# Kernel optimization log

Hardware: AMD Instinct MI355X
Metric: run time of the kernel (lower is better)

The kernel has to match this reference:

```python
import jax, jax.numpy as jnp
import numpy as np
import math

B, S, HID = 1, 4096, 2048
NH, NKV, HD = 16, 4, 128
SKETCH, TOPK = 640, 2048
EPS = 1e-6


def _dct_orthonormal(rows, cols, rng, sink=4, fsink=8):
    i = np.arange(rows)[:, None]
    j = np.arange(cols)[None, :]
    dct = np.cos(np.pi / cols * (j + 0.5) * i)
    dct[0, :] *= math.sqrt(1.0 / cols)
    dct[1:, :] *= math.sqrt(2.0 / cols)
    signs = rng.integers(0, 2, (1, cols)).astype(np.float64) * 2.0 - 1.0
    m = dct * signs
    m[:, :sink] *= 2.0
    m[:fsink, :] *= 1.5
    return m.astype(np.float32)


def setup_inputs() -> dict:
    key = jax.random.key(0)
    ks = jax.random.split(key, 8)
    rng = np.random.default_rng(0)
    # RoPE tables (b, s, 1, head_dim)
    pos = np.arange(S, dtype=np.float32)
    inv = 1.0 / (10000.0 ** (np.arange(0, HD, 2, dtype=np.float32) / HD))
    ang = pos[:, None] * inv[None, :]              # (S, HD/2)
    emb = np.concatenate([ang, ang], axis=-1)       # (S, HD)
    cos = np.broadcast_to(np.cos(emb)[None, :, None, :], (B, S, 1, HD)).copy()
    sin = np.broadcast_to(np.sin(emb)[None, :, None, :], (B, S, 1, HD)).copy()
    w = 0.02
    return {
        'hidden_states': jax.random.normal(ks[0], (B, S, HID), jnp.float32),
        'wq': jax.random.normal(ks[1], (HID, NH * HD), jnp.float32) * w,
        'wk': jax.random.normal(ks[2], (HID, NKV * HD), jnp.float32) * w,
        'wv': jax.random.normal(ks[3], (HID, NKV * HD), jnp.float32) * w,
        'wo': jax.random.normal(ks[4], (NH * HD, HID), jnp.float32) * w,
        'qn_w': jnp.ones((HD,), jnp.float32),
        'kn_w': jnp.ones((HD,), jnp.float32),
        's_w1': jax.random.normal(ks[5], (HID, 64), jnp.float32) * w,
        's_b1': jnp.zeros((64,), jnp.float32),
        's_w2': jax.random.normal(ks[6], (64, 1), jnp.float32) * w,
        's_b2': jnp.zeros((1,), jnp.float32),
        'sketch_scale': jnp.full((1,), 0.1, jnp.float32),
        'kron_a': jnp.asarray(_dct_orthonormal(20, 128, rng)),
        'kron_b': jnp.asarray(_dct_orthonormal(32, 256, rng)),
        'cos': jnp.asarray(cos),
        'sin': jnp.asarray(sin),
    }


def _rms_norm(x, w):
    var = jnp.mean(jnp.square(x), axis=-1, keepdims=True)
    return x * jax.lax.rsqrt(var + EPS) * w


def _rope(x, cos, sin):
    # x: (b, s, h, d); cos/sin: (b, s, 1, d)
    d2 = x.shape[-1] // 2
    rot = jnp.concatenate([-x[..., d2:], x[..., :d2]], axis=-1)
    return x * cos + rot * sin


def reference(hidden_states, wq, wk, wv, wo, qn_w, kn_w, s_w1, s_b1, s_w2, s_b2,
              sketch_scale, kron_a, kron_b, cos, sin):
    b, s, _ = hidden_states.shape
    # importance scorer with compression pressure bias
    logits = jnp.tanh(hidden_states @ s_w1 + s_b1) @ s_w2 + s_b2   # (b, s, 1)
    if s > SKETCH:
        logits = logits - math.log(s / SKETCH)
    iw = jax.nn.sigmoid(logits)                                    # (b, s, 1)

    q = (hidden_states @ wq).reshape(b, s, NH, HD)
    k = (hidden_states @ wk).reshape(b, s, NKV, HD)
    v = (hidden_states @ wv).reshape(b, s, NKV, HD)
    q = _rms_norm(q, qn_w)
    k = _rms_norm(k, kn_w)

    tk = min(s, TOPK)
    _, idx = jax.lax.top_k(logits[..., 0], tk)                     # (b, tk)
    ix = idx[:, :, None, None]
    k_detail = jnp.take_along_axis(k, ix, axis=1)                  # (b, tk, nkv, d)
    v_detail = jnp.take_along_axis(v, ix, axis=1)
    cos_det = jnp.take_along_axis(cos, ix, axis=1)                 # (b, tk, 1, d)
    sin_det = jnp.take_along_axis(sin, ix, axis=1)

    # Kronecker sketch of importance-weighted K/V over all tokens
    P = jnp.kron(kron_a, kron_b)[:, :s]                            # (640, s)
    kw = k * iw[..., None]
    vw = v * iw[..., None]
    k_sketch = jnp.einsum('bshd,ms->bmhd', kw, P) * sketch_scale
    v_sketch = jnp.einsum('bshd,ms->bmhd', vw, P) * sketch_scale

    q_rope = _rope(q, cos, sin)
    k_detail = _rope(k_detail, cos_det, sin_det)

    k_final = jnp.concatenate([k_detail, k_sketch], axis=1)        # (b, tk+640, nkv, d)
    v_final = jnp.concatenate([v_detail, v_sketch], axis=1)
    rep = NH // NKV
    k_final = jnp.repeat(k_final, rep, axis=2)                     # (b, L, nh, d)
    v_final = jnp.repeat(v_final, rep, axis=2)

    scores = jnp.einsum('bqhd,bkhd->bhqk', q_rope, k_final) / math.sqrt(HD)
    attn = jax.nn.softmax(scores, axis=-1)
    out = jnp.einsum('bhqk,bkhd->bqhd', attn, v_final).reshape(b, s, NH * HD)
    return out @ wo
```

## Files before the change

### kernel.cpp

```cpp
#include <hip/hip_runtime.h>
#include <math.h>

typedef _Float16 f16;
typedef f16 f16x8 __attribute__((ext_vector_type(8)));
typedef float f32x4 __attribute__((ext_vector_type(4)));

#define MFMA16(a,b,c) __builtin_amdgcn_mfma_f32_16x16x32_f16(a,b,c,0,0,0)

static __device__ __forceinline__ f16x8 ld8(const f16* p) { return *(const f16x8*)p; }

static __device__ __forceinline__ float exp2a(float x) {
    float r; asm("v_exp_f32 %0, %1" : "=v"(r) : "v"(x)); return r;
}

#if __has_builtin(__builtin_amdgcn_global_load_lds)
#define GLL16(g, lptr) __builtin_amdgcn_global_load_lds((const __attribute__((address_space(1))) void*)(g), (__attribute__((address_space(3))) void*)(lptr), 16, 0, 0)
#else
#define GLL16(g, lptr) do { *(int4*)(lptr) = *(const int4*)(g); } while (0)
#endif

__global__ __launch_bounds__(256) void k_mlp1(const float* __restrict__ h, const float* __restrict__ w1,
                                              double* __restrict__ part, f16* __restrict__ h16) {
    __shared__ float hs[64 * 68];
    __shared__ float ws[64 * 64];
    int rb = blockIdx.x, ks = blockIdx.y;
    int tid = threadIdx.x;
    int jq = tid & 15, rt = tid >> 4;
    double acc[4][4];
    #pragma unroll
    for (int r = 0; r < 4; ++r)
        #pragma unroll
        for (int q = 0; q < 4; ++q) acc[r][q] = 0.0;

    float4 hreg[4], wreg[4];
    int hrow[4], hcq[4], wc[4], wq[4];
    #pragma unroll
    for (int i = 0; i < 4; ++i) {
        int fl = i * 256 + tid;
        hrow[i] = fl >> 4; hcq[i] = fl & 15;
        wc[i] = fl >> 4;   wq[i] = fl & 15;
    }
    #define LOADCH(c8) do {                                                                  \
        _Pragma("unroll")                                                                     \
        for (int i = 0; i < 4; ++i) {                                                         \
            hreg[i] = *(const float4*)&h[(size_t)(rb*64 + hrow[i])*2048 + ks*512 + (c8)*64 + hcq[i]*4]; \
            wreg[i] = *(const float4*)&w1[(size_t)(ks*512 + (c8)*64 + wc[i])*64 + wq[i]*4];   \
        }                                                                                     \
    } while (0)

    LOADCH(0);
    for (int c8 = 0; c8 < 8; ++c8) {
        __syncthreads();
        #pragma unroll
        for (int i = 0; i < 4; ++i) {
            *(float4*)&hs[hrow[i]*68 + hcq[i]*4] = hreg[i];
            *(float4*)&ws[wc[i]*64 + wq[i]*4] = wreg[i];
            const float* hp = (const float*)&hreg[i];
            f16 h4[4];
            #pragma unroll
            for (int z = 0; z < 4; ++z) h4[z] = (f16)hp[z];
            *(float*)&h16[(size_t)(rb*64 + hrow[i])*2048 + ks*512 + c8*64 + hcq[i]*4] = *(float*)h4;
            *(float*)(&h16[(size_t)(rb*64 + hrow[i])*2048 + ks*512 + c8*64 + hcq[i]*4 + 2]) = *(((float*)h4)+1);
        }
        __syncthreads();
        if (c8 < 7) LOADCH(c8 + 1);
        #pragma unroll 4
        for (int cg = 0; cg < 64; cg += 4) {
            float4 ha[4], wa[4];
            #pragma unroll
            for (int r = 0; r < 4; ++r) ha[r] = *(const float4*)&hs[(rt + 16*r)*68 + cg];
            #pragma unroll
            for (int cc = 0; cc < 4; ++cc) wa[cc] = *(const float4*)&ws[(cg + cc)*64 + jq*4];
            #pragma unroll
            for (int cc = 0; cc < 4; ++cc) {
                const float* wap = (const float*)&wa[cc];
                double wd0 = (double)wap[0], wd1 = (double)wap[1], wd2 = (double)wap[2], wd3 = (double)wap[3];
                #pragma unroll
                for (int r = 0; r < 4; ++r) {
                    double hv = (double)((const float*)&ha[r])[cc];
                    acc[r][0] = fma(hv, wd0, acc[r][0]);
                    acc[r][1] = fma(hv, wd1, acc[r][1]);
                    acc[r][2] = fma(hv, wd2, acc[r][2]);
                    acc[r][3] = fma(hv, wd3, acc[r][3]);
                }
            }
        }
    }
    #pragma unroll
    for (int r = 0; r < 4; ++r)
        #pragma unroll
        for (int q = 0; q < 4; ++q)
            part[((size_t)ks*4096 + rb*64 + rt + 16*r)*64 + jq*4 + q] = acc[r][q];
    #undef LOADCH
}

__global__ __launch_bounds__(256) void k_mlp2(const double* __restrict__ part, const float* __restrict__ b1,
                                              const float* __restrict__ w2, const float* __restrict__ b2,
                                              double* __restrict__ logitsD, float* __restrict__ iw) {
    int tid = threadIdx.x;
    int j = tid & 63, rq = tid >> 6;
    int row = blockIdx.x * 4 + rq;
    double s = part[(size_t)row*64 + j] + part[((size_t)4096 + row)*64 + j]
             + part[((size_t)8192 + row)*64 + j] + part[((size_t)12288 + row)*64 + j];
    double t = tanh(s + (double)b1[j]);
    double v = t * (double)w2[j];
    #pragma unroll
    for (int o = 32; o > 0; o >>= 1) v += __shfl_down(v, o);
    if (j == 0) {
        double lg = v + (double)b2[0] - 1.8562979903656263;
        logitsD[row] = lg;
        iw[row] = (float)(1.0 / (1.0 + exp(-lg)));
    }
}

__global__ __launch_bounds__(256) void k_transpose_qkv(const float* __restrict__ wq, const float* __restrict__ wk,
                                                       const float* __restrict__ wv, f16* __restrict__ out) {
    __shared__ float tile[32][33];
    int bx = blockIdx.x;
    const float* in; int inCols, colBase, rowOff;
    if (bx < 64)      { in = wq; inCols = 2048; colBase = bx * 32;        rowOff = colBase; }
    else if (bx < 80) { in = wk; inCols = 512;  colBase = (bx - 64) * 32; rowOff = 2048 + colBase; }
    else              { in = wv; inCols = 512;  colBase = (bx - 80) * 32; rowOff = 2560 + colBase; }
    int tx = threadIdx.x, ty = threadIdx.y;
    int x = colBase + tx;
    int y0 = blockIdx.y * 32;
    #pragma unroll
    for (int i = 0; i < 4; ++i)
        tile[ty + i*8][tx] = in[(size_t)(y0 + ty + i*8) * inCols + x];
    __syncthreads();
    #pragma unroll
    for (int i = 0; i < 4; ++i)
        out[(size_t)(rowOff + ty + i*8) * 2048 + y0 + tx] = (f16)tile[tx][ty + i*8];
}

__global__ __launch_bounds__(256) void k_transpose(const float* __restrict__ in, f16* __restrict__ out,
                                                   int inCols, int rowOff) {
    __shared__ float tile[32][33];
    int tx = threadIdx.x, ty = threadIdx.y;
    int x = blockIdx.x * 32 + tx;
    int y0 = blockIdx.y * 32;
    #pragma unroll
    for (int i = 0; i < 4; ++i)
        tile[ty + i*8][tx] = in[(size_t)(y0 + ty + i*8) * inCols + x];
    __syncthreads();
    #pragma unroll
    for (int i = 0; i < 4; ++i)
        out[(size_t)(rowOff + blockIdx.x*32 + ty + i*8) * 2048 + y0 + tx] = (f16)tile[tx][ty + i*8];
}

__global__ __launch_bounds__(1024) void k_topk(const double* __restrict__ logitsD, int* __restrict__ sel) {
    __shared__ unsigned long long keys[4096];
    __shared__ unsigned int hist[2048];
    __shared__ unsigned int bcast[2];
    __shared__ unsigned int cA, cB;
    int tid = threadIdx.x;
    for (int i = tid; i < 4096; i += 1024) {
        unsigned long long u = (unsigned long long)__double_as_longlong(logitsD[i]);
        keys[i] = (u >> 63) ? ~u : (u | 0x8000000000000000ull);
    }
    if (tid == 0) { cA = 0; cB = 0; }
    unsigned long long Tpart = 0;
    unsigned int need = 2048;
    #pragma unroll 1
    for (int lvl = 0; lvl < 6; ++lvl) {
        int shift = (lvl < 5) ? (53 - 11*lvl) : 0;
        int width = (lvl < 5) ? 11 : 9;
        unsigned int nb = 1u << width;
        int hiShift = shift + width;
        for (int i = tid; i < (int)nb; i += 1024) hist[i] = 0;
        __syncthreads();
        for (int i = tid; i < 4096; i += 1024) {
            unsigned long long k = keys[i];
            bool cand = (lvl == 0) || ((k >> hiShift) == (Tpart >> hiShift));
            if (cand) atomicAdd(&hist[(unsigned int)(k >> shift) & (nb - 1u)], 1u);
        }
        __syncthreads();
        if (tid < 64) {
            int chunk = (int)nb >> 6;
            int base = (int)nb - (tid + 1) * chunk;
            unsigned int sum = 0;
            for (int jj = 0; jj < chunk; ++jj) sum += hist[base + jj];
            unsigned int pre = sum;
            #pragma unroll
            for (int o = 1; o < 64; o <<= 1) {
                unsigned int t = __shfl_up(pre, o);
                if (tid >= o) pre += t;
            }
            unsigned int preEx = pre - sum;
            if (preEx < need && need <= pre) {
                unsigned int cum = preEx;
                for (int jj = chunk - 1; jj >= 0; --jj) {
                    unsigned int c = hist[base + jj];
                    if (cum + c >= need) { bcast[0] = (unsigned int)(base + jj); bcast[1] = need - cum; break; }
                    cum += c;
                }
            }
        }
        __syncthreads();
        Tpart |= ((unsigned long long)bcast[0]) << shift;
        need = bcast[1];
        __syncthreads();
    }
    unsigned int G = 2048 - need;
    for (int i = tid; i < 4096; i += 1024) {
        unsigned long long k = keys[i];
        if (k > Tpart) { unsigned int p = atomicAdd(&cA, 1u); sel[p] = i; }
        else if (k == Tpart) { unsigned int q = atomicAdd(&cB, 1u); if (q < need) sel[G + q] = i; }
    }
}

__global__ __launch_bounds__(256) void k_gemm(const f16* __restrict__ A, const f16* __restrict__ Bt,
                                              float* __restrict__ C, int M, int N, int K) {
    __shared__ f16 As[128 * 32];
    __shared__ f16 Bs[128 * 32];
    int tid = threadIdx.x;
    int w = tid >> 6, l = tid & 63, lr = l & 15, lg = l >> 4;
    int wr = w >> 1, wc = w & 1;
    int row0 = blockIdx.y * 128, col0 = blockIdx.x * 128;
    f32x4 zero = {0.f, 0.f, 0.f, 0.f};
    f32x4 acc[4][4];
    #pragma unroll
    for (int m = 0; m < 4; ++m)
        #pragma unroll
        for (int n = 0; n < 4; ++n) acc[m][n] = zero;
    for (int k0 = 0; k0 < K; k0 += 32) {
        #pragma unroll
        for (int p = 0; p < 2; ++p) {
            int id = p * 256 + tid;
            int r = id >> 2, c8 = (id & 3) * 8;
            GLL16(&A[(size_t)(row0 + r) * K + k0 + c8], &As[id * 8]);
            GLL16(&Bt[(size_t)(col0 + r) * K + k0 + c8], &Bs[id * 8]);
        }
        __syncthreads();
        f16x8 a[4], b[4];
        #pragma unroll
        for (int m = 0; m < 4; ++m) a[m] = ld8(&As[(wr*64 + m*16 + lr) * 32 + lg*8]);
        #pragma unroll
        for (int n = 0; n < 4; ++n) b[n] = ld8(&Bs[(wc*64 + n*16 + lr) * 32 + lg*8]);
        #pragma unroll
        for (int m = 0; m < 4; ++m)
            #pragma unroll
            for (int n = 0; n < 4; ++n)
                acc[m][n] = MFMA16(a[m], b[n], acc[m][n]);
        __syncthreads();
    }
    #pragma unroll
    for (int m = 0; m < 4; ++m)
        #pragma unroll
        for (int n = 0; n < 4; ++n)
            #pragma unroll
            for (int i = 0; i < 4; ++i)
                C[(size_t)(row0 + wr*64 + m*16 + lg*4 + i) * N + col0 + wc*64 + n*16 + lr] = acc[m][n][i];
}

__global__ __launch_bounds__(320) void k_norm(const float* __restrict__ qkv, const float* __restrict__ qnw,
                                              const float* __restrict__ knw, const float* __restrict__ cosb,
                                              const float* __restrict__ sinb, f16* __restrict__ qr,
                                              float* __restrict__ kn) {
    int s = blockIdx.x;
    int tid = threadIdx.x;
    if (tid < 256) {
        int h = tid >> 4, ln = tid & 15, d0 = ln * 8;
        const float* src = &qkv[(size_t)s * 3072 + h * 128 + d0];
        float4 a = *(const float4*)src, b = *(const float4*)(src + 4);
        float x[8] = {a.x,a.y,a.z,a.w,b.x,b.y,b.z,b.w};
        float ss = 0;
        #pragma unroll
        for (int j = 0; j < 8; ++j) ss += x[j]*x[j];
        ss += __shfl_xor(ss,1); ss += __shfl_xor(ss,2); ss += __shfl_xor(ss,4); ss += __shfl_xor(ss,8);
        float rn = rsqrtf(ss * (1.0f/128.0f) + 1e-6f);
        float xn[8];
        #pragma unroll
        for (int j = 0; j < 8; ++j) xn[j] = x[j] * rn * qnw[d0 + j];
        const float scl = 0.088388347648318447f * 1.4426950408889634f;
        f16x8 o;
        #pragma unroll
        for (int j = 0; j < 8; ++j) {
            float pr = __shfl_xor(xn[j], 8);
            float rot = (ln < 8) ? -pr : pr;
            int d = d0 + j;
            o[j] = (f16)((xn[j]*cosb[s*128 + d] + rot*sinb[s*128 + d]) * scl);
        }
        *(f16x8*)&qr[(size_t)s * 2048 + h * 128 + d0] = o;
    } else {
        int t2 = tid - 256;
        int h = t2 >> 4, ln = t2 & 15, d0 = ln * 8;
        const float* src = &qkv[(size_t)s * 3072 + 2048 + h * 128 + d0];
        float4 a = *(const float4*)src, b = *(const float4*)(src + 4);
        float x[8] = {a.x,a.y,a.z,a.w,b.x,b.y,b.z,b.w};
        float ss = 0;
        #pragma unroll
        for (int j = 0; j < 8; ++j) ss += x[j]*x[j];
        ss += __shfl_xor(ss,1); ss += __shfl_xor(ss,2); ss += __shfl_xor(ss,4); ss += __shfl_xor(ss,8);
        float rn = rsqrtf(ss * (1.0f/128.0f) + 1e-6f);
        float o[8];
        #pragma unroll
        for (int j = 0; j < 8; ++j) o[j] = x[j] * rn * knw[d0 + j];
        float* dst = &kn[(size_t)s*512 + h*128 + d0];
        *(float4*)dst = make_float4(o[0],o[1],o[2],o[3]);
        *(float4*)(dst+4) = make_float4(o[4],o[5],o[6],o[7]);
    }
}

__global__ __launch_bounds__(128) void k_gather(const int* __restrict__ sel, const float* __restrict__ kn,
                                                const float* __restrict__ qkv, const float* __restrict__ cosb,
                                                const float* __restrict__ sinb, f16* __restrict__ Kf,
                                                f16* __restrict__ VfT) {
    int j = blockIdx.x;
    int s = sel[j];
    int t = threadIdx.x;
    float c = cosb[s*128 + t], sn = sinb[s*128 + t];
    #pragma unroll
    for (int h = 0; h < 4; ++h) {
        float x  = kn[(size_t)s*512 + h*128 + t];
        float pr = kn[(size_t)s*512 + h*128 + (t ^ 64)];
        float rot = (t < 64) ? -pr : pr;
        Kf[(size_t)(h*2688 + j) * 128 + t] = (f16)(x*c + rot*sn);
        float v = qkv[(size_t)s*3072 + 2560 + h*128 + t];
        VfT[(size_t)h*128*2688 + (size_t)t*2688 + j] = (f16)v;
    }
}

__global__ __launch_bounds__(256) void k_sketch1(const float* __restrict__ kn, const float* __restrict__ qkv,
                                                 const float* __restrict__ iw, const float* __restrict__ kronb,
                                                 float* __restrict__ T) {
    int mb = blockIdx.x & 31, sa = blockIdx.x >> 5;
    int which = blockIdx.y;
    int c0 = threadIdx.x * 2;
    float a0 = 0, a1 = 0;
    for (int sb = 0; sb < 256; ++sb) {
        int s = sa * 256 + sb;
        float wgt = kronb[mb * 256 + sb] * iw[s];
        const float* src = which ? &qkv[(size_t)s*3072 + 2560] : &kn[(size_t)s*512];
        a0 += wgt * src[c0];
        a1 += wgt * src[c0 + 1];
    }
    float* dst = &T[(size_t)((which*32 + mb)*16 + sa) * 512 + c0];
    dst[0] = a0; dst[1] = a1;
}

__global__ __launch_bounds__(256) void k_sketch2(const float* __restrict__ T, const float* __restrict__ krona,
                                                 const float* __restrict__ sscale, f16* __restrict__ Kf,
                                                 f16* __restrict__ VfT) {
    int m = blockIdx.x;
    int which = blockIdx.y;
    int ma = m >> 5, mb = m & 31;
    int c0 = threadIdx.x * 2;
    float sc = sscale[0];
    float a0 = 0, a1 = 0;
    #pragma unroll
    for (int sa = 0; sa < 16; ++sa) {
        float ka = krona[ma * 128 + sa];
        const float* t = &T[(size_t)((which*32 + mb)*16 + sa) * 512 + c0];
        a0 += ka * t[0];
        a1 += ka * t[1];
    }
    a0 *= sc; a1 *= sc;
    int key = 2048 + m;
    int h0 = c0 >> 7, d = c0 & 127;
    if (which == 0) {
        Kf[(size_t)(h0*2688 + key)*128 + d]     = (f16)a0;
        Kf[(size_t)(h0*2688 + key)*128 + d + 1] = (f16)a1;
    } else {
        VfT[(size_t)h0*128*2688 + (size_t)d*2688 + key]       = (f16)a0;
        VfT[(size_t)h0*128*2688 + (size_t)(d+1)*2688 + key]   = (f16)a1;
    }
}

__global__ __launch_bounds__(256, 2) void k_attn(const f16* __restrict__ qr, const f16* __restrict__ Kf,
                                                 const f16* __restrict__ VfT, f16* __restrict__ out16) {
    __shared__ f16 KT[2][64 * 128];
    __shared__ f16 VT[2][128 * 64];
    __shared__ f16 P[4][32 * 64];
    int qt = blockIdx.x, h = blockIdx.y;
    int kvh = h >> 2;
    int tid = threadIdx.x;
    int w = tid >> 6, l = tid & 63, lr = l & 15, lg = l >> 4;
    int q0 = qt * 128 + w * 32;
    const char* Kb = (const char*)(Kf + (size_t)kvh * 2688 * 128);
    const char* Vb = (const char*)(VfT + (size_t)kvh * 128 * 2688);
    char* Pw = (char*)&P[w][0];

    int koff[4], voff[2];
    #pragma unroll
    for (int c = 0; c < 4; ++c) koff[c] = (c*64 + lg*16) ^ ((lr & 7) << 5);
    #pragma unroll
    for (int kw = 0; kw < 2; ++kw) voff[kw] = (kw*64 + lg*16) ^ ((lr & 7) << 4);
    int psw = (lr & 7) << 4;

    int L0 = tid * 16;

    f16x8 aq[2][4];
    #pragma unroll
    for (int hh = 0; hh < 2; ++hh)
        #pragma unroll
        for (int c = 0; c < 4; ++c)
            aq[hh][c] = ld8(&qr[(size_t)(q0 + hh*16 + lr) * 2048 + h*128 + c*32 + lg*8]);

    f32x4 zero = {0.f,0.f,0.f,0.f};
    f32x4 o0[8], o1[8];
    #pragma unroll
    for (int f = 0; f < 8; ++f) { o0[f] = zero; o1[f] = zero; }
    float m0[4], m1[4], ls0[4], ls1[4];
    #pragma unroll
    for (int i = 0; i < 4; ++i) { m0[i] = -1e30f; m1[i] = -1e30f; ls0[i] = 0.f; ls1[i] = 0.f; }

    #define STAGE(buf, kt)  do {                                                          \
        _Pragma("unroll")                                                                  \
        for (int i_ = 0; i_ < 4; ++i_) {                                                   \
            int L = L0 + i_*4096;                                                          \
            int krow = L >> 8, kbc = L & 255;                                              \
            GLL16(Kb + (size_t)((kt) + krow)*256 + (kbc ^ ((krow & 7) << 5)),              \
                  (char*)&KT[buf][0] + L);                                                 \
            int vd = L >> 7, vbc = L & 127;                                                \
            GLL16(Vb + (size_t)vd*5376 + (size_t)(kt)*2 + (vbc ^ ((vd & 7) << 4)),         \
                  (char*)&VT[buf][0] + L);                                                 \
        }                                                                                  \
    } while (0)

    STAGE(0, 0);
    asm volatile("s_waitcnt vmcnt(0)" ::: "memory");
    __syncthreads();

    for (int t = 0; t < 42; ++t) {
        int cur = t & 1;
        if (t < 41) STAGE(cur ^ 1, (t + 1) * 64);
        const char* Kc = (const char*)&KT[cur][0];
        const char* Vc = (const char*)&VT[cur][0];

        f32x4 s0[4], s1[4];
        #pragma unroll
        for (int tt = 0; tt < 4; ++tt) { s0[tt] = zero; s1[tt] = zero; }
        __builtin_amdgcn_s_setprio(1);
        #pragma unroll
        for (int tt = 0; tt < 4; ++tt) {
            #pragma unroll
            for (int c = 0; c < 4; ++c) {
                f16x8 kb = ld8((const f16*)(Kc + (tt*16 + lr)*256 + koff[c]));
                s0[tt] = MFMA16(aq[0][c], kb, s0[tt]);
                s1[tt] = MFMA16(aq[1][c], kb, s1[tt]);
            }
        }
        __builtin_amdgcn_s_setprio(0);

        float tl0[4], tl1[4];
        bool need = false;
        #pragma unroll
        for (int i = 0; i < 4; ++i) {
            tl0[i] = fmaxf(fmaxf(s0[0][i], s0[1][i]), fmaxf(s0[2][i], s0[3][i]));
            tl1[i] = fmaxf(fmaxf(s1[0][i], s1[1][i]), fmaxf(s1[2][i], s1[3][i]));
            need = need || (tl0[i] > m0[i]+8.f) || (tl1[i] > m1[i]+8.f);
        }
        if (__any(need)) {
            f32x4 cf0, cf1;
            #pragma unroll
            for (int i = 0; i < 4; ++i) {
                float a = tl0[i];
                a = fmaxf(a, __shfl_xor(a, 1)); a = fmaxf(a, __shfl_xor(a, 2));
                a = fmaxf(a, __shfl_xor(a, 4)); a = fmaxf(a, __shfl_xor(a, 8));
                float mn0 = fmaxf(m0[i], a);
                cf0[i] = exp2a(m0[i] - mn0); m0[i] = mn0; ls0[i] *= cf0[i];
                float b = tl1[i];
                b = fmaxf(b, __shfl_xor(b, 1)); b = fmaxf(b, __shfl_xor(b, 2));
                b = fmaxf(b, __shfl_xor(b, 4)); b = fmaxf(b, __shfl_xor(b, 8));
                float mn1 = fmaxf(m1[i], b);
                cf1[i] = exp2a(m1[i] - mn1); m1[i] = mn1; ls1[i] *= cf1[i];
            }
            #pragma unroll
            for (int f = 0; f < 8; ++f) { o0[f] *= cf0; o1[f] *= cf1; }
        }
        #pragma unroll
        for (int tt = 0; tt < 4; ++tt)
            #pragma unroll
            for (int i = 0; i < 4; ++i) {
                int r0 = lg*4 + i;
                float p0 = exp2a(s0[tt][i] - m0[i]);
                ls0[i] += p0;
                *(f16*)(Pw + ((r0*128 + (tt*16+lr)*2) ^ ((r0 & 7) << 4))) = (f16)p0;
                int r1 = 16 + r0;
                float p1 = exp2a(s1[tt][i] - m1[i]);
                ls1[i] += p1;
                *(f16*)(Pw + ((r1*128 + (tt*16+lr)*2) ^ ((r1 & 7) << 4))) = (f16)p1;
            }
        asm volatile("s_waitcnt lgkmcnt(0)" ::: "memory");
        __builtin_amdgcn_sched_barrier(0);

        __builtin_amdgcn_s_setprio(1);
        #pragma unroll
        for (int kw = 0; kw < 2; ++kw) {
            f16x8 pa0 = *(const f16x8*)(Pw + ((lr*128 + kw*64 + lg*16) ^ psw));
            f16x8 pa1 = *(const f16x8*)(Pw + (((16+lr)*128 + kw*64 + lg*16) ^ psw));
            #pragma unroll
            for (int f = 0; f < 8; ++f) {
                f16x8 vb = ld8((const f16*)(Vc + (f*16 + lr)*128 + voff[kw]));
                o0[f] = MFMA16(pa0, vb, o0[f]);
                o1[f] = MFMA16(pa1, vb, o1[f]);
            }
        }
        __builtin_amdgcn_s_setprio(0);
        asm volatile("s_waitcnt vmcnt(0)" ::: "memory");
        __syncthreads();
    }

    #pragma unroll
    for (int i = 0; i < 4; ++i) {
        float a = ls0[i];
        a += __shfl_xor(a, 1); a += __shfl_xor(a, 2); a += __shfl_xor(a, 4); a += __shfl_xor(a, 8);
        float inv0 = 1.0f / a;
        float b = ls1[i];
        b += __shfl_xor(b, 1); b += __shfl_xor(b, 2); b += __shfl_xor(b, 4); b += __shfl_xor(b, 8);
        float inv1 = 1.0f / b;
        #pragma unroll
        for (int f = 0; f < 8; ++f) {
            out16[(size_t)(q0 + lg*4 + i) * 2048 + h*128 + f*16 + lr]      = (f16)(o0[f][i] * inv0);
            out16[(size_t)(q0 + 16 + lg*4 + i) * 2048 + h*128 + f*16 + lr] = (f16)(o1[f][i] * inv1);
        }
    }
    #undef STAGE
}

extern "C" void kernel_launch(void* const* d_in, const int* in_sizes, int n_in,
                              void* d_out, int out_size, void* d_ws, size_t ws_size,
                              hipStream_t stream) {
    const float* h     = (const float*)d_in[0];
    const float* wq    = (const float*)d_in[1];
    const float* wk    = (const float*)d_in[2];
    const float* wv    = (const float*)d_in[3];
    const float* wo    = (const float*)d_in[4];
    const float* qnw   = (const float*)d_in[5];
    const float* knw   = (const float*)d_in[6];
    const float* sw1   = (const float*)d_in[7];
    const float* sb1   = (const float*)d_in[8];
    const float* sw2   = (const float*)d_in[9];
    const float* sb2   = (const float*)d_in[10];
    const float* sscal = (const float*)d_in[11];
    const float* ka    = (const float*)d_in[12];
    const float* kb    = (const float*)d_in[13];
    const float* cosb  = (const float*)d_in[14];
    const float* sinb  = (const float*)d_in[15];
    float* outp = (float*)d_out;

    char* ws = (char*)d_ws;
    size_t off = 0;
    f16*    h16    = (f16*)(ws + off);   off += (size_t)4096*2048*2;
    f16*    wqkvt  = (f16*)(ws + off);   off += (size_t)3072*2048*2;
    f16*    wot    = (f16*)(ws + off);   off += (size_t)2048*2048*2;
    float*  qkvraw = (float*)(ws + off); off += (size_t)4096*3072*4;
    f16*    qr     = (f16*)(ws + off);   off += (size_t)4096*2048*2;
    float*  kn     = (float*)(ws + off); off += (size_t)4096*512*4;
    f16*    attn16 = (f16*)(ws + off);   off += (size_t)4096*2048*2;
    float*  T      = (float*)(ws + off); off += (size_t)2*32*16*512*4;
    f16*    Kf     = (f16*)(ws + off);   off += (size_t)4*2688*128*2;
    f16*    VfT    = (f16*)(ws + off);   off += (size_t)4*128*2688*2;
    double* logitsD= (double*)(ws + off);off += (size_t)4096*8;
    float*  iw     = (float*)(ws + off); off += (size_t)4096*4;
    int*    sel    = (int*)(ws + off);   off += (size_t)2048*4;
    double* part   = (double*)qkvraw;

    k_mlp1<<<dim3(64,4), 256, 0, stream>>>(h, sw1, part, h16);
    k_mlp2<<<1024, 256, 0, stream>>>(part, sb1, sw2, sb2, logitsD, iw);
    k_transpose_qkv<<<dim3(96,64), dim3(32,8), 0, stream>>>(wq, wk, wv, wqkvt);
    k_transpose<<<dim3(64,64), dim3(32,8), 0, stream>>>(wo, wot, 2048, 0);
    k_topk<<<1, 1024, 0, stream>>>(logitsD, sel);
    k_gemm<<<dim3(24,32), 256, 0, stream>>>(h16, wqkvt, qkvraw, 4096, 3072, 2048);
    k_norm<<<4096, 320, 0, stream>>>(qkvraw, qnw, knw, cosb, sinb, qr, kn);
    k_gather<<<2048, 128, 0, stream>>>(sel, kn, qkvraw, cosb, sinb, Kf, VfT);
    k_sketch1<<<dim3(512,2), 256, 0, stream>>>(kn, qkvraw, iw, kb, T);
    k_sketch2<<<dim3(640,2), 256, 0, stream>>>(T, ka, sscal, Kf, VfT);
    k_attn<<<dim3(32,16), 256, 0, stream>>>(qr, Kf, VfT, attn16);
    k_gemm<<<dim3(16,32), 256, 0, stream>>>(attn16, wot, outp, 4096, 2048, 2048);
}
```

Baseline: 415.7 us.

## Switch attention to 32x32 MFMA with register-resident P and restructure sketch1

The attention kernel is rewritten to use 32x32x16 MFMA computing S^T (K as A operand, Q as B), so each lane owns one query column. The softmax row max and sum then need only a single cross-half shuffle, and P is repacked to f16 in registers via lane shuffles instead of round-tripping through LDS. The K staging swizzle is changed to match the new read pattern. Separately, sketch1 now has each thread accumulate all 32 kron_b rows for one channel, reusing each loaded activation across them but launching only 64 blocks, which risks low occupancy and parallelism.

```diff
diff --git a/kernel.cpp b/kernel.cpp
--- a/kernel.cpp
+++ b/kernel.cpp
@@ -4,13 +4,19 @@
 typedef _Float16 f16;
 typedef f16 f16x8 __attribute__((ext_vector_type(8)));
 typedef float f32x4 __attribute__((ext_vector_type(4)));
+typedef float f32x16 __attribute__((ext_vector_type(16)));
 
 #define MFMA16(a,b,c) __builtin_amdgcn_mfma_f32_16x16x32_f16(a,b,c,0,0,0)
+#define MFMA32(a,b,c) __builtin_amdgcn_mfma_f32_32x32x16_f16(a,b,c,0,0,0)
 
 static __device__ __forceinline__ f16x8 ld8(const f16* p) { return *(const f16x8*)p; }
 
 static __device__ __forceinline__ float exp2a(float x) {
     float r; asm("v_exp_f32 %0, %1" : "=v"(r) : "v"(x)); return r;
+}
+
+static __device__ __forceinline__ unsigned pkh(float x, float y) {
+    union { f16 h[2]; unsigned u; } z; z.h[0] = (f16)x; z.h[1] = (f16)y; return z.u;
 }
 
 #if __has_builtin(__builtin_amdgcn_global_load_lds)
@@ -324,19 +330,21 @@
 __global__ __launch_bounds__(256) void k_sketch1(const float* __restrict__ kn, const float* __restrict__ qkv,
                                                  const float* __restrict__ iw, const float* __restrict__ kronb,
                                                  float* __restrict__ T) {
-    int mb = blockIdx.x & 31, sa = blockIdx.x >> 5;
-    int which = blockIdx.y;
-    int c0 = threadIdx.x * 2;
-    float a0 = 0, a1 = 0;
+    int sa = blockIdx.x, ch = blockIdx.y, which = blockIdx.z;
+    int c = ch * 256 + threadIdx.x;
+    float acc[32];
+    #pragma unroll
+    for (int mb = 0; mb < 32; ++mb) acc[mb] = 0.f;
     for (int sb = 0; sb < 256; ++sb) {
         int s = sa * 256 + sb;
-        float wgt = kronb[mb * 256 + sb] * iw[s];
-        const float* src = which ? &qkv[(size_t)s*3072 + 2560] : &kn[(size_t)s*512];
-        a0 += wgt * src[c0];
-        a1 += wgt * src[c0 + 1];
-    }
-    float* dst = &T[(size_t)((which*32 + mb)*16 + sa) * 512 + c0];
-    dst[0] = a0; dst[1] = a1;
+        float x = (which ? qkv[(size_t)s*3072 + 2560 + c] : kn[(size_t)s*512 + c]) * iw[s];
+        #pragma unroll
+        for (int mb = 0; mb < 32; ++mb)
+            acc[mb] = fmaf(kronb[mb*256 + sb], x, acc[mb]);
+    }
+    #pragma unroll
+    for (int mb = 0; mb < 32; ++mb)
+        T[(size_t)((which*32 + mb)*16 + sa) * 512 + c] = acc[mb];
 }
 
 __global__ __launch_bounds__(256) void k_sketch2(const float* __restrict__ T, const float* __restrict__ krona,
@@ -371,46 +379,36 @@
                                                  const f16* __restrict__ VfT, f16* __restrict__ out16) {
     __shared__ f16 KT[2][64 * 128];
     __shared__ f16 VT[2][128 * 64];
-    __shared__ f16 P[4][32 * 64];
+    __shared__ float bc[4][32];
     int qt = blockIdx.x, h = blockIdx.y;
     int kvh = h >> 2;
     int tid = threadIdx.x;
-    int w = tid >> 6, l = tid & 63, lr = l & 15, lg = l >> 4;
+    int w = tid >> 6, l = tid & 63;
+    int l31 = l & 31, hi = l >> 5;
+    bool lo = (hi == 0);
     int q0 = qt * 128 + w * 32;
     const char* Kb = (const char*)(Kf + (size_t)kvh * 2688 * 128);
     const char* Vb = (const char*)(VfT + (size_t)kvh * 128 * 2688);
-    char* Pw = (char*)&P[w][0];
-
-    int koff[4], voff[2];
-    #pragma unroll
-    for (int c = 0; c < 4; ++c) koff[c] = (c*64 + lg*16) ^ ((lr & 7) << 5);
-    #pragma unroll
-    for (int kw = 0; kw < 2; ++kw) voff[kw] = (kw*64 + lg*16) ^ ((lr & 7) << 4);
-    int psw = (lr & 7) << 4;
-
+    int swz = (l31 & 7) << 4;
     int L0 = tid * 16;
 
-    f16x8 aq[2][4];
-    #pragma unroll
-    for (int hh = 0; hh < 2; ++hh)
-        #pragma unroll
-        for (int c = 0; c < 4; ++c)
-            aq[hh][c] = ld8(&qr[(size_t)(q0 + hh*16 + lr) * 2048 + h*128 + c*32 + lg*8]);
-
-    f32x4 zero = {0.f,0.f,0.f,0.f};
-    f32x4 o0[8], o1[8];
-    #pragma unroll
-    for (int f = 0; f < 8; ++f) { o0[f] = zero; o1[f] = zero; }
-    float m0[4], m1[4], ls0[4], ls1[4];
-    #pragma unroll
-    for (int i = 0; i < 4; ++i) { m0[i] = -1e30f; m1[i] = -1e30f; ls0[i] = 0.f; ls1[i] = 0.f; }
+    f16x8 qf[8];
+    const f16* qp = &qr[(size_t)(q0 + l31) * 2048 + h * 128];
+    #pragma unroll
+    for (int t16 = 0; t16 < 8; ++t16) qf[t16] = ld8(qp + t16*16 + hi*8);
+
+    f32x16 z16 = {0.f};
+    f32x16 o[4];
+    #pragma unroll
+    for (int dt = 0; dt < 4; ++dt) o[dt] = z16;
+    float m = -1e30f, ls = 0.f;
 
     #define STAGE(buf, kt)  do {                                                          \
         _Pragma("unroll")                                                                  \
         for (int i_ = 0; i_ < 4; ++i_) {                                                   \
             int L = L0 + i_*4096;                                                          \
             int krow = L >> 8, kbc = L & 255;                                              \
-            GLL16(Kb + (size_t)((kt) + krow)*256 + (kbc ^ ((krow & 7) << 5)),              \
+            GLL16(Kb + (size_t)((kt) + krow)*256 + (kbc ^ ((krow & 7) << 4)),              \
                   (char*)&KT[buf][0] + L);                                                 \
             int vd = L >> 7, vbc = L & 127;                                                \
             GLL16(Vb + (size_t)vd*5376 + (size_t)(kt)*2 + (vbc ^ ((vd & 7) << 4)),         \
@@ -418,6 +416,15 @@
         }                                                                                  \
     } while (0)
 
+    #define MKPA(dst, P, rho) do {                                                         \
+        unsigned a0 = pkh(P[rho+0], P[rho+1]), a1 = pkh(P[rho+2], P[rho+3]);               \
+        unsigned b0 = pkh(P[rho+4], P[rho+5]), b1 = pkh(P[rho+6], P[rho+7]);               \
+        unsigned as0 = __shfl_xor(a0, 32), as1 = __shfl_xor(a1, 32);                       \
+        unsigned bs0 = __shfl_xor(b0, 32), bs1 = __shfl_xor(b1, 32);                       \
+        dst.u[0] = lo ? a0 : bs0; dst.u[1] = lo ? a1 : bs1;                                \
+        dst.u[2] = lo ? as0 : b0; dst.u[3] = lo ? as1 : b1;                                \
+    } while (0)
+
     STAGE(0, 0);
     asm volatile("s_waitcnt vmcnt(0)" ::: "memory");
     __syncthreads();
@@ -428,73 +435,53 @@
         const char* Kc = (const char*)&KT[cur][0];
         const char* Vc = (const char*)&VT[cur][0];
 
-        f32x4 s0[4], s1[4];
-        #pragma unroll
-        for (int tt = 0; tt < 4; ++tt) { s0[tt] = zero; s1[tt] = zero; }
+        f32x16 s0 = z16, s1 = z16;
         __builtin_amdgcn_s_setprio(1);
         #pragma unroll
-        for (int tt = 0; tt < 4; ++tt) {
-            #pragma unroll
-            for (int c = 0; c < 4; ++c) {
-                f16x8 kb = ld8((const f16*)(Kc + (tt*16 + lr)*256 + koff[c]));
-                s0[tt] = MFMA16(aq[0][c], kb, s0[tt]);
-                s1[tt] = MFMA16(aq[1][c], kb, s1[tt]);
+        for (int kt16 = 0; kt16 < 8; ++kt16) {
+            f16x8 kb0 = ld8((const f16*)(Kc + l31*256 + ((kt16*32 + hi*16) ^ swz)));
+            s0 = MFMA32(kb0, qf[kt16], s0);
+            f16x8 kb1 = ld8((const f16*)(Kc + (32 + l31)*256 + ((kt16*32 + hi*16) ^ swz)));
+            s1 = MFMA32(kb1, qf[kt16], s1);
+        }
+        __builtin_amdgcn_s_setprio(0);
+
+        float tm = fmaxf(s0[0], s1[0]);
+        #pragma unroll
+        for (int r = 1; r < 16; ++r) tm = fmaxf(tm, fmaxf(s0[r], s1[r]));
+        if (__any(tm > m + 8.f)) {
+            float tmf = fmaxf(tm, __shfl_xor(tm, 32));
+            float mn = fmaxf(m, tmf);
+            float cf = exp2a(m - mn);
+            m = mn; ls *= cf;
+            bc[w][l31] = cf;
+            asm volatile("s_waitcnt lgkmcnt(0)" ::: "memory");
+            #pragma unroll
+            for (int r = 0; r < 16; ++r) {
+                float c2 = bc[w][(r&3) + 8*(r>>2) + 4*hi];
+                #pragma unroll
+                for (int dt = 0; dt < 4; ++dt) o[dt][r] *= c2;
             }
         }
-        __builtin_amdgcn_s_setprio(0);
-
-        float tl0[4], tl1[4];
-        bool need = false;
-        #pragma unroll
-        for (int i = 0; i < 4; ++i) {
-            tl0[i] = fmaxf(fmaxf(s0[0][i], s0[1][i]), fmaxf(s0[2][i], s0[3][i]));
-            tl1[i] = fmaxf(fmaxf(s1[0][i], s1[1][i]), fmaxf(s1[2][i], s1[3][i]));
-            need = need || (tl0[i] > m0[i]+8.f) || (tl1[i] > m1[i]+8.f);
-        }
-        if (__any(need)) {
-            f32x4 cf0, cf1;
-            #pragma unroll
-            for (int i = 0; i < 4; ++i) {
-                float a = tl0[i];
-                a = fmaxf(a, __shfl_xor(a, 1)); a = fmaxf(a, __shfl_xor(a, 2));
-                a = fmaxf(a, __shfl_xor(a, 4)); a = fmaxf(a, __shfl_xor(a, 8));
-                float mn0 = fmaxf(m0[i], a);
-                cf0[i] = exp2a(m0[i] - mn0); m0[i] = mn0; ls0[i] *= cf0[i];
-                float b = tl1[i];
-                b = fmaxf(b, __shfl_xor(b, 1)); b = fmaxf(b, __shfl_xor(b, 2));
-                b = fmaxf(b, __shfl_xor(b, 4)); b = fmaxf(b, __shfl_xor(b, 8));
-                float mn1 = fmaxf(m1[i], b);
-                cf1[i] = exp2a(m1[i] - mn1); m1[i] = mn1; ls1[i] *= cf1[i];
-            }
-            #pragma unroll
-            for (int f = 0; f < 8; ++f) { o0[f] *= cf0; o1[f] *= cf1; }
-        }
-        #pragma unroll
-        for (int tt = 0; tt < 4; ++tt)
-            #pragma unroll
-            for (int i = 0; i < 4; ++i) {
-                int r0 = lg*4 + i;
-                float p0 = exp2a(s0[tt][i] - m0[i]);
-                ls0[i] += p0;
-                *(f16*)(Pw + ((r0*128 + (tt*16+lr)*2) ^ ((r0 & 7) << 4))) = (f16)p0;
-                int r1 = 16 + r0;
-                float p1 = exp2a(s1[tt][i] - m1[i]);
-                ls1[i] += p1;
-                *(f16*)(Pw + ((r1*128 + (tt*16+lr)*2) ^ ((r1 & 7) << 4))) = (f16)p1;
-            }
-        asm volatile("s_waitcnt lgkmcnt(0)" ::: "memory");
-        __builtin_amdgcn_sched_barrier(0);
+        float lsa = 0.f, lsb = 0.f;
+        #pragma unroll
+        for (int r = 0; r < 16; ++r) {
+            s0[r] = exp2a(s0[r] - m); lsa += s0[r];
+            s1[r] = exp2a(s1[r] - m); lsb += s1[r];
+        }
+        ls += lsa + lsb;
+
+        union PA { unsigned u[4]; f16x8 v; } pa[4];
+        MKPA(pa[0], s0, 0); MKPA(pa[1], s0, 8);
+        MKPA(pa[2], s1, 0); MKPA(pa[3], s1, 8);
 
         __builtin_amdgcn_s_setprio(1);
         #pragma unroll
-        for (int kw = 0; kw < 2; ++kw) {
-            f16x8 pa0 = *(const f16x8*)(Pw + ((lr*128 + kw*64 + lg*16) ^ psw));
-            f16x8 pa1 = *(const f16x8*)(Pw + (((16+lr)*128 + kw*64 + lg*16) ^ psw));
-            #pragma unroll
-            for (int f = 0; f < 8; ++f) {
-                f16x8 vb = ld8((const f16*)(Vc + (f*16 + lr)*128 + voff[kw]));
-                o0[f] = MFMA16(pa0, vb, o0[f]);
-                o1[f] = MFMA16(pa1, vb, o1[f]);
+        for (int dt = 0; dt < 4; ++dt) {
+            #pragma unroll
+            for (int sl = 0; sl < 4; ++sl) {
+                f16x8 vb = ld8((const f16*)(Vc + (dt*32 + l31)*128 + ((sl*32 + hi*16) ^ swz)));
+                o[dt] = MFMA32(pa[sl].v, vb, o[dt]);
             }
         }
         __builtin_amdgcn_s_setprio(0);
@@ -502,21 +489,20 @@
         __syncthreads();
     }
 
-    #pragma unroll
-    for (int i = 0; i < 4; ++i) {
-        float a = ls0[i];
-        a += __shfl_xor(a, 1); a += __shfl_xor(a, 2); a += __shfl_xor(a, 4); a += __shfl_xor(a, 8);
-        float inv0 = 1.0f / a;
-        float b = ls1[i];
-        b += __shfl_xor(b, 1); b += __shfl_xor(b, 2); b += __shfl_xor(b, 4); b += __shfl_xor(b, 8);
-        float inv1 = 1.0f / b;
-        #pragma unroll
-        for (int f = 0; f < 8; ++f) {
-            out16[(size_t)(q0 + lg*4 + i) * 2048 + h*128 + f*16 + lr]      = (f16)(o0[f][i] * inv0);
-            out16[(size_t)(q0 + 16 + lg*4 + i) * 2048 + h*128 + f*16 + lr] = (f16)(o1[f][i] * inv1);
-        }
+    float lst = ls + __shfl_xor(ls, 32);
+    float inv = 1.0f / lst;
+    bc[w][l31] = inv;
+    asm volatile("s_waitcnt lgkmcnt(0)" ::: "memory");
+    #pragma unroll
+    for (int r = 0; r < 16; ++r) {
+        int q = (r&3) + 8*(r>>2) + 4*hi;
+        float iv = bc[w][q];
+        #pragma unroll
+        for (int dt = 0; dt < 4; ++dt)
+            out16[(size_t)(q0 + q) * 2048 + h*128 + dt*32 + l31] = (f16)(o[dt][r] * iv);
     }
     #undef STAGE
+    #undef MKPA
 }
 
 extern "C" void kernel_launch(void* const* d_in, const int* in_sizes, int n_in,
@@ -565,7 +551,7 @@
     k_gemm<<<dim3(24,32), 256, 0, stream>>>(h16, wqkvt, qkvraw, 4096, 3072, 2048);
     k_norm<<<4096, 320, 0, stream>>>(qkvraw, qnw, knw, cosb, sinb, qr, kn);
     k_gather<<<2048, 128, 0, stream>>>(sel, kn, qkvraw, cosb, sinb, Kf, VfT);
-    k_sketch1<<<dim3(512,2), 256, 0, stream>>>(kn, qkvraw, iw, kb, T);
+    k_sketch1<<<dim3(16,2,2), 256, 0, stream>>>(kn, qkvraw, iw, kb, T);
     k_sketch2<<<dim3(640,2), 256, 0, stream>>>(T, ka, sscal, Kf, VfT);
     k_attn<<<dim3(32,16), 256, 0, stream>>>(qr, Kf, VfT, attn16);
     k_gemm<<<dim3(16,32), 256, 0, stream>>>(attn16, wot, outp, 4096, 2048, 2048);
```

Result: slower. 459.4 us (+10.5%).
